# Optimization experiments

Hardware: AMD Instinct MI355X
Metric: run time of the kernel (lower is better)

The kernel has to match this reference:

```python
import jax, jax.numpy as jnp
import numpy as np
from jax import lax

DIM = 64
HEADS = 8
B, H, W = 4, 256, 256


def layer_norm(x, w, b):
    # WithBias LayerNorm over channel dim (dim=1 of NCHW), per-pixel
    mu = jnp.mean(x, axis=1, keepdims=True)
    var = jnp.mean((x - mu) ** 2, axis=1, keepdims=True)
    xn = (x - mu) / jnp.sqrt(var + 1e-5)
    return xn * w[None, :, None, None] + b[None, :, None, None]


def conv1x1(x, w, b=None):
    out = jnp.einsum('oc,bchw->bohw', w, x)
    if b is not None:
        out = out + b[None, :, None, None]
    return out


def dwconv3x3(x, w):
    # w: [C,1,3,3], depthwise (groups=C), stride 1, pad 1
    return lax.conv_general_dilated(
        x, w, window_strides=(1, 1), padding=((1, 1), (1, 1)),
        feature_group_count=x.shape[1],
        dimension_numbers=('NCHW', 'OIHW', 'NCHW'))


def modulation(v, y, mw, mb):
    # mw: [4, C, C] = [scale0, scale1, shift0, shift1]; mb: [4, C]
    s = conv1x1(jax.nn.leaky_relu(conv1x1(y, mw[0], mb[0]), 0.1), mw[1], mb[1])
    t = conv1x1(jax.nn.leaky_relu(conv1x1(y, mw[2], mb[2]), 0.1), mw[3], mb[3])
    return v * (s + 1.0) + t


def _heads(t):
    b, c, h, w = t.shape
    return t.reshape(b, HEADS, c // HEADS, h * w)


def channel_attn(q, k, v, temp):
    b, c, h, w = v.shape
    q, k, v = _heads(q), _heads(k), _heads(v)  # b, head, ch, hw
    q = q / jnp.maximum(jnp.linalg.norm(q, axis=-1, keepdims=True), 1e-12)
    k = k / jnp.maximum(jnp.linalg.norm(k, axis=-1, keepdims=True), 1e-12)
    attn = jnp.einsum('bhcn,bhdn->bhcd', q, k) * temp[None]  # small CxC
    attn = jax.nn.softmax(attn, axis=-1)
    out = jnp.einsum('bhcd,bhdn->bhcn', attn, v)
    return out.reshape(b, c, h, w)


def setup_inputs() -> dict:
    key = jax.random.key(0)
    ks = jax.random.split(key, 24)
    sc = 0.05
    d = {
        'x': jax.random.normal(ks[0], (B, DIM, H, W), jnp.float32),
        'y': jax.random.normal(ks[1], (B, DIM, H, W), jnp.float32),
        'ln_w': jnp.ones((DIM,), jnp.float32),
        'ln_b': jnp.zeros((DIM,), jnp.float32),
        'temp': jnp.ones((HEADS, 1, 1), jnp.float32),
        'kv1_w': jax.random.normal(ks[2], (2 * DIM, DIM), jnp.float32) * sc,
        'kvdw1_w': jax.random.normal(ks[3], (2 * DIM, 1, 3, 3), jnp.float32) * sc,
        'q1_w': jax.random.normal(ks[4], (DIM, DIM), jnp.float32) * sc,
        'qdw1_w': jax.random.normal(ks[5], (DIM, 1, 3, 3), jnp.float32) * sc,
        'po1_w': jax.random.normal(ks[6], (DIM, DIM), jnp.float32) * sc,
        'kv2_w': jax.random.normal(ks[7], (2 * DIM, DIM), jnp.float32) * sc,
        'kvdw2_w': jax.random.normal(ks[8], (2 * DIM, 1, 3, 3), jnp.float32) * sc,
        'q2_w': jax.random.normal(ks[9], (DIM, DIM), jnp.float32) * sc,
        'qdw2_w': jax.random.normal(ks[10], (DIM, 1, 3, 3), jnp.float32) * sc,
        'po2_w': jax.random.normal(ks[11], (DIM, DIM), jnp.float32) * sc,
        'mm1_w': jax.random.normal(ks[12], (4, DIM, DIM), jnp.float32) * sc,
        'mm1_b': jnp.zeros((4, DIM), jnp.float32),
        'mm2_w': jax.random.normal(ks[13], (4, DIM, DIM), jnp.float32) * sc,
        'mm2_b': jnp.zeros((4, DIM), jnp.float32),
    }
    return d


def reference(x, y, ln_w, ln_b, temp,
              kv1_w, kvdw1_w, q1_w, qdw1_w, po1_w,
              kv2_w, kvdw2_w, q2_w, qdw2_w, po2_w,
              mm1_w, mm1_b, mm2_w, mm2_b):
    x1 = layer_norm(x, ln_w, ln_b)
    y1 = layer_norm(y, ln_w, ln_b)  # original reuses self.norm1 for both

    # branch 1: kv from x1, q from y1, v modulated by x, residual y
    kv1 = dwconv3x3(conv1x1(x1, kv1_w), kvdw1_w)
    k1, v1 = jnp.split(kv1, 2, axis=1)
    q1 = dwconv3x3(conv1x1(y1, q1_w), qdw1_w)
    v1 = modulation(v1, x, mm1_w, mm1_b)
    out1 = conv1x1(channel_attn(q1, k1, v1, temp), po1_w) + y

    # branch 2: kv from y1, q from x1, v modulated by y, residual x
    kv2 = dwconv3x3(conv1x1(y1, kv2_w), kvdw2_w)
    k2, v2 = jnp.split(kv2, 2, axis=1)
    q2 = dwconv3x3(conv1x1(x1, q2_w), qdw2_w)
    v2 = modulation(v2, y, mm2_w, mm2_b)
    out2 = conv1x1(channel_attn(q2, k2, v2, temp), po2_w) + x

    return (out1, out2)
```

## Files before the change

kernel.cpp:

```cpp
#include <hip/hip_runtime.h>
#include <hip/hip_bf16.h>

#define HW 65536
#define BATCH 4
#define NPIX (BATCH*HW)

typedef unsigned short u16;
typedef unsigned int   u32;
typedef __attribute__((ext_vector_type(8))) short bh8;
typedef __attribute__((ext_vector_type(4))) float f4;

__device__ __forceinline__ float b2f(u16 u){
    u32 i = ((u32)u) << 16; float f; __builtin_memcpy(&f, &i, 4); return f;
}
__device__ __forceinline__ u16 f2b(float f){
    __hip_bfloat16 h = __float2bfloat16(f); u16 u; __builtin_memcpy(&u, &h, 2); return u;
}

__device__ __forceinline__ f4 mfma16(bh8 a, bh8 b, f4 c){
    return __builtin_amdgcn_mfma_f32_16x16x32_bf16(a, b, c, 0, 0, 0);
}

struct CvtJob { const float* src; u16* dst; int n; const float* cs; };
struct SetupArgs {
    CvtJob j[12];
    const float* kvw[2]; const float* qw[2];
    const float* lnw; const float* lnb;
    float* sums; float* lnc;
};
__global__ __launch_bounds__(256) void setup_kernel(SetupArgs S){
    int blk = blockIdx.x;
    if (blk < 12){
        const CvtJob J = S.j[blk];
        if (J.cs){
            for (int i = threadIdx.x; i < J.n; i += 256) J.dst[i] = f2b(J.src[i] * J.cs[i & 63]);
        } else {
            for (int i = threadIdx.x; i < J.n; i += 256) J.dst[i] = f2b(J.src[i]);
        }
        return;
    }
    int pb = blk - 12;
    if (pb == 0){
        for (int i = threadIdx.x; i < 5120; i += 256) S.sums[i] = 0.f;
    } else if (pb <= 2){
        const float* W = S.kvw[pb-1];
        float* rs = S.lnc + (pb-1)*256;
        int o = threadIdx.x;
        if (o < 128){
            float a = 0.f, bb = 0.f;
            for (int c = 0; c < 64; c++){
                float wv = W[o*64 + c];
                a = fmaf(wv, S.lnw[c], a); bb = fmaf(wv, S.lnb[c], bb);
            }
            rs[o] = a; rs[128 + o] = bb;
        }
    } else {
        const float* W = S.qw[pb-3];
        float* rs = S.lnc + 512 + (pb-3)*128;
        int o = threadIdx.x;
        if (o < 64){
            float a = 0.f, bb = 0.f;
            for (int c = 0; c < 64; c++){
                float wv = W[o*64 + c];
                a = fmaf(wv, S.lnw[c], a); bb = fmaf(wv, S.lnb[c], bb);
            }
            rs[o] = a; rs[64 + o] = bb;
        }
    }
}

struct GemmDual {
    const float* in[2];
    const u16* wa[2];
    const float* rs[2]; const float* rb[2];
    u16* outLo[2]; u16* outHi[2];
};
template<int MT>
__global__ __launch_bounds__(256,4) void gemmln_kernel(GemmDual G){
    constexpr int KD = 64;
    constexpr int NW = MT*16*KD;
    __shared__ u16 wl[NW];
    int seg = blockIdx.x >> 11, tile = blockIdx.x & 2047;
    {
        const u16* W = G.wa[seg];
        for (int i = threadIdx.x; i < NW/8; i += 256){
            int row = i >> 3, ch = i & 7;
            uint4 v = *(const uint4*)(W + row*KD + ch*8);
            *(uint4*)(wl + row*KD + ((ch ^ (row & 7)) << 3)) = v;
        }
    }
    __syncthreads();

    int w = threadIdx.x >> 6, lane = threadIdx.x & 63;
    int quad = lane >> 4, l16 = lane & 15;
    int b = tile >> 9;
    int pbase = ((tile & 511) << 7) + (w << 5) + (l16 << 1);

    f4 acc[MT][2];
    #pragma unroll
    for (int mi = 0; mi < MT; mi++){ acc[mi][0] = (f4){0.f,0.f,0.f,0.f}; acc[mi][1] = (f4){0.f,0.f,0.f,0.f}; }

    float s1a = 0.f, s2a = 0.f, s1b = 0.f, s2b = 0.f;
    #pragma unroll
    for (int ks = 0; ks < 2; ks++){
        const float* pp = G.in[seg] + ((size_t)b*64 + ks*32 + quad*8)*HW + pbase;
        bh8 b0, b1;
        #pragma unroll
        for (int j = 0; j < 8; j++){
            float2 f = *(const float2*)(pp + (size_t)j*HW);
            s1a += f.x; s2a = fmaf(f.x, f.x, s2a);
            s1b += f.y; s2b = fmaf(f.y, f.y, s2b);
            b0[j] = (short)f2b(f.x);
            b1[j] = (short)f2b(f.y);
        }
        #pragma unroll
        for (int mi = 0; mi < MT; mi++){
            bh8 a;
            __builtin_memcpy(&a, wl + (mi*16 + l16)*KD + ((((ks<<2)+quad) ^ (l16 & 7)) << 3), 16);
            acc[mi][0] = mfma16(a, b0, acc[mi][0]);
            acc[mi][1] = mfma16(a, b1, acc[mi][1]);
        }
    }

    s1a += __shfl_xor(s1a, 16); s1a += __shfl_xor(s1a, 32);
    s2a += __shfl_xor(s2a, 16); s2a += __shfl_xor(s2a, 32);
    s1b += __shfl_xor(s1b, 16); s1b += __shfl_xor(s1b, 32);
    s2b += __shfl_xor(s2b, 16); s2b += __shfl_xor(s2b, 32);
    float mu0 = s1a*(1.f/64.f), iv0 = rsqrtf(s2a*(1.f/64.f) - mu0*mu0 + 1e-5f);
    float mu1 = s1b*(1.f/64.f), iv1 = rsqrtf(s2b*(1.f/64.f) - mu1*mu1 + 1e-5f);

    const float* rs = G.rs[seg]; const float* rb = G.rb[seg];
    u16* oLo = G.outLo[seg]; u16* oHi = G.outHi[seg];
    #pragma unroll
    for (int mi = 0; mi < MT; mi++)
    #pragma unroll
    for (int r = 0; r < 4; r++){
        int o = mi*16 + quad*4 + r;
        size_t pidx = ((size_t)b*64 + (o & 63))*HW + pbase;
        float rsv = rs[o], rbv = rb[o];
        float va0 = iv0*(acc[mi][0][r] - mu0*rsv) + rbv;
        float va1 = iv1*(acc[mi][1][r] - mu1*rsv) + rbv;
        u16* dst = (o < 64) ? oLo : oHi;
        *(u32*)(dst + pidx) = (u32)f2b(va0) | ((u32)f2b(va1) << 16);
    }
}

struct DwArgs { const u16* in0; const u16* in1; const u16* in2;
                u16* out0; u16* out1; u16* out2;
                const float* w0; const float* w1; const float* w2;
                int c0, c1, c2; };
__global__ __launch_bounds__(256) void dw3_kernel(DwArgs A){
    int seg = blockIdx.x >> 13;
    int lid = ((blockIdx.x & 8191) << 8) + threadIdx.x;
    const u16* inp = seg == 0 ? A.in0 : seg == 1 ? A.in1 : A.in2;
    u16* outp      = seg == 0 ? A.out0 : seg == 1 ? A.out1 : A.out2;
    const float* wd = seg == 0 ? A.w0 : seg == 1 ? A.w1 : A.w2;
    int choff      = seg == 0 ? A.c0 : seg == 1 ? A.c1 : A.c2;
    int bc = lid >> 13;
    int n8 = lid & 8191;
    int h = n8 >> 5, c8 = (n8 & 31) << 3;
    const float* wc = wd + ((size_t)((bc & 63) + choff))*9;
    const u16* p = inp + (size_t)bc*HW;
    float row[3][10];
    #pragma unroll
    for (int r = 0; r < 3; r++){
        int hh = h - 1 + r;
        bool ok = (unsigned)hh < 256u;
        const u16* pr = p + hh*256 + c8;
        if (ok){
            uint4 m = *(const uint4*)pr;
            row[r][1] = b2f((u16)m.x); row[r][2] = b2f((u16)(m.x>>16));
            row[r][3] = b2f((u16)m.y); row[r][4] = b2f((u16)(m.y>>16));
            row[r][5] = b2f((u16)m.z); row[r][6] = b2f((u16)(m.z>>16));
            row[r][7] = b2f((u16)m.w); row[r][8] = b2f((u16)(m.w>>16));
            row[r][0] = (c8 > 0)   ? b2f(pr[-1]) : 0.f;
            row[r][9] = (c8 < 248) ? b2f(pr[8])  : 0.f;
        } else {
            #pragma unroll
            for (int j = 0; j < 10; j++) row[r][j] = 0.f;
        }
    }
    float o[8];
    #pragma unroll
    for (int i = 0; i < 8; i++){
        float a = 0.f;
        #pragma unroll
        for (int r = 0; r < 3; r++){
            a = fmaf(wc[r*3+0], row[r][i],   a);
            a = fmaf(wc[r*3+1], row[r][i+1], a);
            a = fmaf(wc[r*3+2], row[r][i+2], a);
        }
        o[i] = a;
    }
    uint4 st;
    st.x = (u32)f2b(o[0]) | ((u32)f2b(o[1])<<16);
    st.y = (u32)f2b(o[2]) | ((u32)f2b(o[3])<<16);
    st.z = (u32)f2b(o[4]) | ((u32)f2b(o[5])<<16);
    st.w = (u32)f2b(o[6]) | ((u32)f2b(o[7])<<16);
    *(uint4*)(outp + (size_t)bc*HW + h*256 + c8) = st;
}

#define NSL 64
struct AttnDual { const u16* q[2]; const u16* k[2]; float* sums; };
__global__ __launch_bounds__(256) void attn_part_kernel(AttnDual AD){
    int seg = blockIdx.x >> 11;
    int blk = blockIdx.x & 2047;
    int sl = blk & (NSL-1);
    int bh = blk >> 6;
    int b = bh >> 3, h = bh & 7;
    const u16* qp = AD.q[seg] + ((size_t)b*64 + h*8)*HW + sl*(HW/NSL);
    const u16* kp = AD.k[seg] + ((size_t)b*64 + h*8)*HW + sl*(HW/NSL);
    float acc[80];
    #pragma unroll
    for (int i = 0; i < 80; i++) acc[i] = 0.f;
    int n0 = threadIdx.x << 2;
    float qv[8][4], kw[8][4];
    #pragma unroll
    for (int i = 0; i < 8; i++){
        uint2 mq = *(const uint2*)(qp + (size_t)i*HW + n0);
        uint2 mk = *(const uint2*)(kp + (size_t)i*HW + n0);
        qv[i][0] = b2f((u16)(mq.x & 0xffffu)); qv[i][1] = b2f((u16)(mq.x >> 16));
        qv[i][2] = b2f((u16)(mq.y & 0xffffu)); qv[i][3] = b2f((u16)(mq.y >> 16));
        kw[i][0] = b2f((u16)(mk.x & 0xffffu)); kw[i][1] = b2f((u16)(mk.x >> 16));
        kw[i][2] = b2f((u16)(mk.y & 0xffffu)); kw[i][3] = b2f((u16)(mk.y >> 16));
    }
    #pragma unroll
    for (int i = 0; i < 8; i++){
        #pragma unroll
        for (int u = 0; u < 4; u++){
            acc[64+i] = fmaf(qv[i][u], qv[i][u], acc[64+i]);
            acc[72+i] = fmaf(kw[i][u], kw[i][u], acc[72+i]);
        }
        #pragma unroll
        for (int j = 0; j < 8; j++)
            #pragma unroll
            for (int u = 0; u < 4; u++)
                acc[i*8+j] = fmaf(qv[i][u], kw[j][u], acc[i*8+j]);
    }
    __shared__ float sred[4][80];
    int lane = threadIdx.x & 63, wv = threadIdx.x >> 6;
    #pragma unroll
    for (int t = 0; t < 80; t++){
        float r = acc[t];
        r += __shfl_down(r, 32); r += __shfl_down(r, 16); r += __shfl_down(r, 8);
        r += __shfl_down(r, 4);  r += __shfl_down(r, 2);  r += __shfl_down(r, 1);
        if (lane == 0) sred[wv][t] = r;
    }
    __syncthreads();
    if (threadIdx.x < 80){
        int t = threadIdx.x;
        atomicAdd(&AD.sums[seg*2560 + bh*80 + t], sred[0][t]+sred[1][t]+sred[2][t]+sred[3][t]);
    }
}

struct WeffDual { const float* sums; const float* temp; const float* po[2]; u16* weff[2]; };
__global__ __launch_bounds__(64) void weff_kernel(WeffDual WD){
    int seg = blockIdx.x >> 2;
    int b = blockIdx.x & 3;
    const float* po = WD.po[seg];
    u16* weff = WD.weff[seg];
    __shared__ float at[8][8][8];
    int t = threadIdx.x;
    {
        int h = t >> 3, i = t & 7;
        const float* f = WD.sums + seg*2560 + (b*8 + h)*80;
        float iq = 1.f / fmaxf(sqrtf(f[64+i]), 1e-12f);
        float tv = WD.temp[h];
        float row[8]; float m = -1e30f;
        #pragma unroll
        for (int j = 0; j < 8; j++){
            float ik = 1.f / fmaxf(sqrtf(f[72+j]), 1e-12f);
            row[j] = f[i*8+j]*iq*ik*tv;
            m = fmaxf(m, row[j]);
        }
        float s = 0.f;
        #pragma unroll
        for (int j = 0; j < 8; j++){ row[j] = expf(row[j]-m); s += row[j]; }
        float rsv = 1.f/s;
        #pragma unroll
        for (int j = 0; j < 8; j++) at[h][i][j] = row[j]*rsv;
    }
    __syncthreads();
    int o = t;
    for (int g = 0; g < 64; g++){
        int h = g >> 3, j = g & 7;
        float wv = 0.f;
        #pragma unroll
        for (int i = 0; i < 8; i++) wv = fmaf(po[o*64 + h*8 + i], at[h][i][j], wv);
        weff[b*4096 + o*64 + g] = f2b(wv);
    }
}

struct ModFinal {
    const float* in[2]; const u16* wa[2]; const u16* wb[2];
    const float* b0[2]; const float* b2[2]; const float* b1[2]; const float* b3[2];
    const u16* wf[2];
    const u16* v[2];
    const float* resid[2];
    float* out[2];
};
__global__ __launch_bounds__(256) void modfinal_kernel(ModFinal M){
    __shared__ u32 lds[128*65];
    __shared__ u16 wl[8192];
    int seg = blockIdx.x >> 11, tile = blockIdx.x & 2047;
    int w = threadIdx.x >> 6, lane = threadIdx.x & 63;
    int quad = lane >> 4, l16 = lane & 15;
    int b = tile >> 9;
    int pbase = ((tile & 511) << 7) + (w << 5) + (l16 << 1);
    int pxp = (w << 4) + l16;

    auto loadW = [&](const u16* W, int nrows){
        for (int i = threadIdx.x; i < nrows*8; i += 256){
            int row = i >> 3, ch = i & 7;
            uint4 vv = *(const uint4*)(W + row*64 + ch*8);
            *(uint4*)(wl + row*64 + ((ch ^ (row & 7)) << 3)) = vv;
        }
    };

    loadW(M.wa[seg], 128);
    __syncthreads();
    f4 acc[8][2];
    #pragma unroll
    for (int mi = 0; mi < 8; mi++){ acc[mi][0] = (f4){0.f,0.f,0.f,0.f}; acc[mi][1] = (f4){0.f,0.f,0.f,0.f}; }
    #pragma unroll
    for (int ks = 0; ks < 2; ks++){
        const float* pp = M.in[seg] + ((size_t)b*64 + ks*32 + quad*8)*HW + pbase;
        bh8 f0, f1;
        #pragma unroll
        for (int j = 0; j < 8; j++){
            float2 f = *(const float2*)(pp + (size_t)j*HW);
            f0[j] = (short)f2b(f.x);
            f1[j] = (short)f2b(f.y);
        }
        #pragma unroll
        for (int mi = 0; mi < 8; mi++){
            bh8 a;
            __builtin_memcpy(&a, wl + (mi*16 + l16)*64 + ((((ks<<2)+quad) ^ (l16 & 7)) << 3), 16);
            acc[mi][0] = mfma16(a, f0, acc[mi][0]);
            acc[mi][1] = mfma16(a, f1, acc[mi][1]);
        }
    }
    {
        const float* b0v = M.b0[seg]; const float* b2v = M.b2[seg];
        #pragma unroll
        for (int mi = 0; mi < 8; mi++)
        #pragma unroll
        for (int r = 0; r < 4; r++){
            int o = mi*16 + quad*4 + r;
            float bi = (o < 64) ? b0v[o] : b2v[o-64];
            float v0 = acc[mi][0][r] + bi; v0 = v0 > 0.f ? v0 : 0.1f*v0;
            float v1 = acc[mi][1][r] + bi; v1 = v1 > 0.f ? v1 : 0.1f*v1;
            lds[o*65 + ((pxp + ((o>>2)&3)*4) & 63)] = (u32)f2b(v0) | ((u32)f2b(v1) << 16);
        }
    }
    __syncthreads();

    loadW(M.wb[seg], 128);
    __syncthreads();
    f4 acc2[8][2];
    #pragma unroll
    for (int mi = 0; mi < 8; mi++){ acc2[mi][0] = (f4){0.f,0.f,0.f,0.f}; acc2[mi][1] = (f4){0.f,0.f,0.f,0.f}; }
    #pragma unroll
    for (int ks = 0; ks < 4; ks++){
        int kb = ks*32 + quad*8;
        bh8 bb0, bb1;
        #pragma unroll
        for (int j = 0; j < 8; j++){
            int ch = kb + j;
            u32 m = lds[ch*65 + ((pxp + ((ch>>2)&3)*4) & 63)];
            bb0[j] = (short)(m & 0xffffu);
            bb1[j] = (short)(m >> 16);
        }
        #pragma unroll
        for (int mi = 0; mi < 8; mi++){
            if (mi < 4 ? (ks < 2) : (ks >= 2)){
                int ksl = (mi >= 4) ? ks - 2 : ks;
                bh8 a;
                __builtin_memcpy(&a, wl + (mi*16 + l16)*64 + ((((ksl<<2)+quad) ^ (l16 & 7)) << 3), 16);
                acc2[mi][0] = mfma16(a, bb0, acc2[mi][0]);
                acc2[mi][1] = mfma16(a, bb1, acc2[mi][1]);
            }
        }
    }
    __syncthreads();

    loadW(M.wf[seg] + b*4096, 64);
    {
        const float* b1v = M.b1[seg]; const float* b3v = M.b3[seg];
        const u16* vP = M.v[seg];
        #pragma unroll
        for (int mi = 0; mi < 4; mi++)
        #pragma unroll
        for (int r = 0; r < 4; r++){
            int o = mi*16 + quad*4 + r;
            size_t pidx = ((size_t)b*64 + o)*HW + pbase;
            float s0 = acc2[mi][0][r] + b1v[o];
            float s1 = acc2[mi][1][r] + b1v[o];
            float t0 = acc2[mi+4][0][r] + b3v[o];
            float t1 = acc2[mi+4][1][r] + b3v[o];
            u32 vv = *(const u32*)(vP + pidx);
            float v0 = b2f((u16)(vv & 0xffffu)), v1 = b2f((u16)(vv >> 16));
            lds[o*65 + ((pxp + ((o>>2)&3)*4) & 63)] = (u32)f2b(v0*(s0+1.f)+t0)
                                                    | ((u32)f2b(v1*(s1+1.f)+t1) << 16);
        }
    }
    __syncthreads();

    f4 accF[4][2];
    #pragma unroll
    for (int mi = 0; mi < 4; mi++){ accF[mi][0] = (f4){0.f,0.f,0.f,0.f}; accF[mi][1] = (f4){0.f,0.f,0.f,0.f}; }
    #pragma unroll
    for (int ks = 0; ks < 2; ks++){
        int kb = ks*32 + quad*8;
        bh8 bb0, bb1;
        #pragma unroll
        for (int j = 0; j < 8; j++){
            int ch = kb + j;
            u32 m = lds[ch*65 + ((pxp + ((ch>>2)&3)*4) & 63)];
            bb0[j] = (short)(m & 0xffffu);
            bb1[j] = (short)(m >> 16);
        }
        #pragma unroll
        for (int mi = 0; mi < 4; mi++){
            bh8 a;
            __builtin_memcpy(&a, wl + (mi*16 + l16)*64 + ((((ks<<2)+quad) ^ (l16 & 7)) << 3), 16);
            accF[mi][0] = mfma16(a, bb0, accF[mi][0]);
            accF[mi][1] = mfma16(a, bb1, accF[mi][1]);
        }
    }
    {
        const float* resid = M.resid[seg];
        float* outF = M.out[seg];
        #pragma unroll
        for (int mi = 0; mi < 4; mi++)
        #pragma unroll
        for (int r = 0; r < 4; r++){
            int o = mi*16 + quad*4 + r;
            size_t pidx = ((size_t)b*64 + o)*HW + pbase;
            float2 rr = *(const float2*)(resid + pidx);
            float2 st; st.x = accF[mi][0][r] + rr.x; st.y = accF[mi][1][r] + rr.y;
            *(float2*)(outF + pidx) = st;
        }
    }
}

extern "C" void kernel_launch(void* const* d_in, const int* in_sizes, int n_in,
                              void* d_out, int out_size, void* d_ws, size_t ws_size,
                              hipStream_t stream){
    const float* x    = (const float*)d_in[0];
    const float* y    = (const float*)d_in[1];
    const float* ln_w = (const float*)d_in[2];
    const float* ln_b = (const float*)d_in[3];
    const float* temp = (const float*)d_in[4];
    const float* kv_w[2]   = {(const float*)d_in[5],  (const float*)d_in[10]};
    const float* kvdw_w[2] = {(const float*)d_in[6],  (const float*)d_in[11]};
    const float* q_w[2]    = {(const float*)d_in[7],  (const float*)d_in[12]};
    const float* qdw_w[2]  = {(const float*)d_in[8],  (const float*)d_in[13]};
    const float* po_w[2]   = {(const float*)d_in[9],  (const float*)d_in[14]};
    const float* mm_w[2]   = {(const float*)d_in[15], (const float*)d_in[17]};
    const float* mm_b[2]   = {(const float*)d_in[16], (const float*)d_in[18]};

    const size_t HPE = (size_t)BATCH*64*HW;
    u16* PL = (u16*)d_ws;
    u16* P[9];
    for (int i = 0; i < 9; i++) P[i] = PL + (size_t)i*HPE;
    float* sums = (float*)(PL + 9*HPE);
    float* lnc  = sums + 5120;
    u16* warena = (u16*)(lnc + 768);
    const int WKV[2] = {0, 8192}, WQ[2] = {16384, 20480};
    const int WMA[2] = {24576, 40960}, WMB[2] = {32768, 49152};
    const int WEFF[2] = {57344, 73728};

    size_t need = 9*HPE*2 + (5120+768)*4 + 90112*2;
    if (ws_size < need) return;

    SetupArgs S{};
    int nj = 0;
    auto add = [&](const float* s, u16* d, int n, const float* cs){ S.j[nj] = {s, d, n, cs}; nj++; };
    for (int br = 0; br < 2; br++){
        add(kv_w[br],        warena + WKV[br],        8192, ln_w);
        add(q_w[br],         warena + WQ[br],         4096, ln_w);
        add(mm_w[br],        warena + WMA[br],        4096, nullptr);
        add(mm_w[br]+8192,   warena + WMA[br] + 4096, 4096, nullptr);
        add(mm_w[br]+4096,   warena + WMB[br],        4096, nullptr);
        add(mm_w[br]+12288,  warena + WMB[br] + 4096, 4096, nullptr);
    }
    S.kvw[0] = kv_w[0]; S.kvw[1] = kv_w[1];
    S.qw[0]  = q_w[0];  S.qw[1]  = q_w[1];
    S.lnw = ln_w; S.lnb = ln_b; S.sums = sums; S.lnc = lnc;
    setup_kernel<<<17, 256, 0, stream>>>(S);

    const int GT = NPIX/128;

    GemmDual GK{};
    GK.in[0] = x; GK.in[1] = y;
    GK.wa[0] = warena + WKV[0]; GK.wa[1] = warena + WKV[1];
    GK.rs[0] = lnc;        GK.rb[0] = lnc + 128;
    GK.rs[1] = lnc + 256;  GK.rb[1] = lnc + 384;
    GK.outLo[0] = P[0]; GK.outHi[0] = P[1];
    GK.outLo[1] = P[3]; GK.outHi[1] = P[4];
    gemmln_kernel<8><<<2*GT, 256, 0, stream>>>(GK);

    GemmDual GQ{};
    GQ.in[0] = y; GQ.in[1] = x;
    GQ.wa[0] = warena + WQ[0]; GQ.wa[1] = warena + WQ[1];
    GQ.rs[0] = lnc + 512;  GQ.rb[0] = lnc + 576;
    GQ.rs[1] = lnc + 640;  GQ.rb[1] = lnc + 704;
    GQ.outLo[0] = P[2]; GQ.outHi[0] = P[2];
    GQ.outLo[1] = P[5]; GQ.outHi[1] = P[5];
    gemmln_kernel<4><<<2*GT, 256, 0, stream>>>(GQ);

    DwArgs D0{P[0], P[1], P[2], P[6], P[7], P[8],
              kvdw_w[0], kvdw_w[0], qdw_w[0], 0, 64, 0};
    dw3_kernel<<<3*8192, 256, 0, stream>>>(D0);
    DwArgs D1{P[3], P[4], P[5], P[0], P[1], P[2],
              kvdw_w[1], kvdw_w[1], qdw_w[1], 0, 64, 0};
    dw3_kernel<<<3*8192, 256, 0, stream>>>(D1);

    AttnDual AD{};
    AD.q[0] = P[8]; AD.k[0] = P[6];
    AD.q[1] = P[2]; AD.k[1] = P[0];
    AD.sums = sums;
    attn_part_kernel<<<2*BATCH*8*NSL, 256, 0, stream>>>(AD);

    WeffDual WD{};
    WD.sums = sums; WD.temp = temp;
    WD.po[0] = po_w[0]; WD.po[1] = po_w[1];
    WD.weff[0] = warena + WEFF[0]; WD.weff[1] = warena + WEFF[1];
    weff_kernel<<<2*BATCH, 64, 0, stream>>>(WD);

    float* outp = (float*)d_out;
    ModFinal M{};
    M.in[0] = x; M.in[1] = y;
    M.wa[0] = warena + WMA[0]; M.wa[1] = warena + WMA[1];
    M.wb[0] = warena + WMB[0]; M.wb[1] = warena + WMB[1];
    M.b0[0] = mm_b[0];       M.b0[1] = mm_b[1];
    M.b2[0] = mm_b[0] + 128; M.b2[1] = mm_b[1] + 128;
    M.b1[0] = mm_b[0] + 64;  M.b1[1] = mm_b[1] + 64;
    M.b3[0] = mm_b[0] + 192; M.b3[1] = mm_b[1] + 192;
    M.wf[0] = warena + WEFF[0]; M.wf[1] = warena + WEFF[1];
    M.v[0] = P[7]; M.v[1] = P[1];
    M.resid[0] = y; M.resid[1] = x;
    M.out[0] = outp; M.out[1] = outp + HPE;
    modfinal_kernel<<<2*GT, 256, 0, stream>>>(M);
}
```

Baseline: 741.5 us.

## Prefetch inputs early, read weights from global, merge depthwise launches

The LN-GEMM kernel now issues all input loads before staging weights into LDS, so global latency overlaps the weight copy. The modulation/final kernel drops its LDS weight staging and reads MFMA A-fragments straight from global/L1. It also double-buffers the input loads and prefetches the v and residual values ahead of the syncs, and shrinks the padded LDS tile to 128x64 with a new swizzle so it can run at higher occupancy. The two depthwise launches become one six-segment launch, which needs three more workspace planes and reassigned buffers. The trade-off is more register pressure from the prefetch arrays and uncoalesced global weight reads.

```diff
diff --git a/kernel.cpp b/kernel.cpp
--- a/kernel.cpp
+++ b/kernel.cpp
@@ -81,6 +81,19 @@
     constexpr int NW = MT*16*KD;
     __shared__ u16 wl[NW];
     int seg = blockIdx.x >> 11, tile = blockIdx.x & 2047;
+    int w = threadIdx.x >> 6, lane = threadIdx.x & 63;
+    int quad = lane >> 4, l16 = lane & 15;
+    int b = tile >> 9;
+    int pbase = ((tile & 511) << 7) + (w << 5) + (l16 << 1);
+
+    const float* in = G.in[seg];
+    float2 f[16];
+    #pragma unroll
+    for (int ks = 0; ks < 2; ks++)
+        #pragma unroll
+        for (int j = 0; j < 8; j++)
+            f[ks*8+j] = *(const float2*)(in + ((size_t)b*64 + ks*32 + quad*8 + j)*HW + pbase);
+
     {
         const u16* W = G.wa[seg];
         for (int i = threadIdx.x; i < NW/8; i += 256){
@@ -91,36 +104,31 @@
     }
     __syncthreads();
 
-    int w = threadIdx.x >> 6, lane = threadIdx.x & 63;
-    int quad = lane >> 4, l16 = lane & 15;
-    int b = tile >> 9;
-    int pbase = ((tile & 511) << 7) + (w << 5) + (l16 << 1);
+    float s1a = 0.f, s2a = 0.f, s1b = 0.f, s2b = 0.f;
+    bh8 b0[2], b1[2];
+    #pragma unroll
+    for (int ks = 0; ks < 2; ks++)
+        #pragma unroll
+        for (int j = 0; j < 8; j++){
+            float2 fv = f[ks*8+j];
+            s1a += fv.x; s2a = fmaf(fv.x, fv.x, s2a);
+            s1b += fv.y; s2b = fmaf(fv.y, fv.y, s2b);
+            b0[ks][j] = (short)f2b(fv.x);
+            b1[ks][j] = (short)f2b(fv.y);
+        }
 
     f4 acc[MT][2];
     #pragma unroll
     for (int mi = 0; mi < MT; mi++){ acc[mi][0] = (f4){0.f,0.f,0.f,0.f}; acc[mi][1] = (f4){0.f,0.f,0.f,0.f}; }
-
-    float s1a = 0.f, s2a = 0.f, s1b = 0.f, s2b = 0.f;
-    #pragma unroll
-    for (int ks = 0; ks < 2; ks++){
-        const float* pp = G.in[seg] + ((size_t)b*64 + ks*32 + quad*8)*HW + pbase;
-        bh8 b0, b1;
-        #pragma unroll
-        for (int j = 0; j < 8; j++){
-            float2 f = *(const float2*)(pp + (size_t)j*HW);
-            s1a += f.x; s2a = fmaf(f.x, f.x, s2a);
-            s1b += f.y; s2b = fmaf(f.y, f.y, s2b);
-            b0[j] = (short)f2b(f.x);
-            b1[j] = (short)f2b(f.y);
-        }
+    #pragma unroll
+    for (int ks = 0; ks < 2; ks++)
         #pragma unroll
         for (int mi = 0; mi < MT; mi++){
             bh8 a;
             __builtin_memcpy(&a, wl + (mi*16 + l16)*KD + ((((ks<<2)+quad) ^ (l16 & 7)) << 3), 16);
-            acc[mi][0] = mfma16(a, b0, acc[mi][0]);
-            acc[mi][1] = mfma16(a, b1, acc[mi][1]);
-        }
-    }
+            acc[mi][0] = mfma16(a, b0[ks], acc[mi][0]);
+            acc[mi][1] = mfma16(a, b1[ks], acc[mi][1]);
+        }
 
     s1a += __shfl_xor(s1a, 16); s1a += __shfl_xor(s1a, 32);
     s2a += __shfl_xor(s2a, 16); s2a += __shfl_xor(s2a, 32);
@@ -145,17 +153,14 @@
     }
 }
 
-struct DwArgs { const u16* in0; const u16* in1; const u16* in2;
-                u16* out0; u16* out1; u16* out2;
-                const float* w0; const float* w1; const float* w2;
-                int c0, c1, c2; };
-__global__ __launch_bounds__(256) void dw3_kernel(DwArgs A){
+struct Dw6 { const u16* in[6]; u16* out[6]; const float* w[6]; int choff[6]; };
+__global__ __launch_bounds__(256) void dw6_kernel(Dw6 A){
     int seg = blockIdx.x >> 13;
     int lid = ((blockIdx.x & 8191) << 8) + threadIdx.x;
-    const u16* inp = seg == 0 ? A.in0 : seg == 1 ? A.in1 : A.in2;
-    u16* outp      = seg == 0 ? A.out0 : seg == 1 ? A.out1 : A.out2;
-    const float* wd = seg == 0 ? A.w0 : seg == 1 ? A.w1 : A.w2;
-    int choff      = seg == 0 ? A.c0 : seg == 1 ? A.c1 : A.c2;
+    const u16* inp = A.in[seg];
+    u16* outp      = A.out[seg];
+    const float* wd = A.w[seg];
+    int choff      = A.choff[seg];
     int bc = lid >> 13;
     int n8 = lid & 8191;
     int h = n8 >> 5, c8 = (n8 & 31) << 3;
@@ -299,9 +304,8 @@
     const float* resid[2];
     float* out[2];
 };
-__global__ __launch_bounds__(256) void modfinal_kernel(ModFinal M){
-    __shared__ u32 lds[128*65];
-    __shared__ u16 wl[8192];
+__global__ __launch_bounds__(256,4) void modfinal_kernel(ModFinal M){
+    __shared__ u32 lds[128*64];
     int seg = blockIdx.x >> 11, tile = blockIdx.x & 2047;
     int w = threadIdx.x >> 6, lane = threadIdx.x & 63;
     int quad = lane >> 4, l16 = lane & 15;
@@ -309,37 +313,53 @@
     int pbase = ((tile & 511) << 7) + (w << 5) + (l16 << 1);
     int pxp = (w << 4) + l16;
 
-    auto loadW = [&](const u16* W, int nrows){
-        for (int i = threadIdx.x; i < nrows*8; i += 256){
-            int row = i >> 3, ch = i & 7;
-            uint4 vv = *(const uint4*)(W + row*64 + ch*8);
-            *(uint4*)(wl + row*64 + ((ch ^ (row & 7)) << 3)) = vv;
-        }
-    };
-
-    loadW(M.wa[seg], 128);
-    __syncthreads();
+    const float* in = M.in[seg];
+    const u16* wa = M.wa[seg];
+
+    float2 f[8];
+    #pragma unroll
+    for (int j = 0; j < 8; j++)
+        f[j] = *(const float2*)(in + ((size_t)b*64 + quad*8 + j)*HW + pbase);
+
     f4 acc[8][2];
     #pragma unroll
     for (int mi = 0; mi < 8; mi++){ acc[mi][0] = (f4){0.f,0.f,0.f,0.f}; acc[mi][1] = (f4){0.f,0.f,0.f,0.f}; }
+
     #pragma unroll
     for (int ks = 0; ks < 2; ks++){
-        const float* pp = M.in[seg] + ((size_t)b*64 + ks*32 + quad*8)*HW + pbase;
+        float2 fn[8];
+        if (ks == 0){
+            #pragma unroll
+            for (int j = 0; j < 8; j++)
+                fn[j] = *(const float2*)(in + ((size_t)b*64 + 32 + quad*8 + j)*HW + pbase);
+        }
         bh8 f0, f1;
         #pragma unroll
         for (int j = 0; j < 8; j++){
-            float2 f = *(const float2*)(pp + (size_t)j*HW);
-            f0[j] = (short)f2b(f.x);
-            f1[j] = (short)f2b(f.y);
+            f0[j] = (short)f2b(f[j].x);
+            f1[j] = (short)f2b(f[j].y);
         }
         #pragma unroll
         for (int mi = 0; mi < 8; mi++){
             bh8 a;
-            __builtin_memcpy(&a, wl + (mi*16 + l16)*64 + ((((ks<<2)+quad) ^ (l16 & 7)) << 3), 16);
+            __builtin_memcpy(&a, wa + (mi*16 + l16)*64 + ks*32 + quad*8, 16);
             acc[mi][0] = mfma16(a, f0, acc[mi][0]);
             acc[mi][1] = mfma16(a, f1, acc[mi][1]);
         }
-    }
+        #pragma unroll
+        for (int j = 0; j < 8; j++) f[j] = fn[j];
+    }
+
+    u32 vpref[16];
+    {
+        const u16* vP = M.v[seg];
+        #pragma unroll
+        for (int mi = 0; mi < 4; mi++)
+        #pragma unroll
+        for (int r = 0; r < 4; r++)
+            vpref[mi*4+r] = *(const u32*)(vP + ((size_t)b*64 + mi*16 + quad*4 + r)*HW + pbase);
+    }
+
     {
         const float* b0v = M.b0[seg]; const float* b2v = M.b2[seg];
         #pragma unroll
@@ -350,13 +370,12 @@
             float bi = (o < 64) ? b0v[o] : b2v[o-64];
             float v0 = acc[mi][0][r] + bi; v0 = v0 > 0.f ? v0 : 0.1f*v0;
             float v1 = acc[mi][1][r] + bi; v1 = v1 > 0.f ? v1 : 0.1f*v1;
-            lds[o*65 + ((pxp + ((o>>2)&3)*4) & 63)] = (u32)f2b(v0) | ((u32)f2b(v1) << 16);
+            lds[o*64 + ((pxp + ((o>>2)&3)*8) & 63)] = (u32)f2b(v0) | ((u32)f2b(v1) << 16);
         }
     }
     __syncthreads();
 
-    loadW(M.wb[seg], 128);
-    __syncthreads();
+    const u16* wb = M.wb[seg];
     f4 acc2[8][2];
     #pragma unroll
     for (int mi = 0; mi < 8; mi++){ acc2[mi][0] = (f4){0.f,0.f,0.f,0.f}; acc2[mi][1] = (f4){0.f,0.f,0.f,0.f}; }
@@ -367,7 +386,7 @@
         #pragma unroll
         for (int j = 0; j < 8; j++){
             int ch = kb + j;
-            u32 m = lds[ch*65 + ((pxp + ((ch>>2)&3)*4) & 63)];
+            u32 m = lds[ch*64 + ((pxp + ((ch>>2)&3)*8) & 63)];
             bb0[j] = (short)(m & 0xffffu);
             bb1[j] = (short)(m >> 16);
         }
@@ -376,7 +395,7 @@
             if (mi < 4 ? (ks < 2) : (ks >= 2)){
                 int ksl = (mi >= 4) ? ks - 2 : ks;
                 bh8 a;
-                __builtin_memcpy(&a, wl + (mi*16 + l16)*64 + ((((ksl<<2)+quad) ^ (l16 & 7)) << 3), 16);
+                __builtin_memcpy(&a, wb + (mi*16 + l16)*64 + ksl*32 + quad*8, 16);
                 acc2[mi][0] = mfma16(a, bb0, acc2[mi][0]);
                 acc2[mi][1] = mfma16(a, bb1, acc2[mi][1]);
             }
@@ -384,28 +403,35 @@
     }
     __syncthreads();
 
-    loadW(M.wf[seg] + b*4096, 64);
     {
         const float* b1v = M.b1[seg]; const float* b3v = M.b3[seg];
-        const u16* vP = M.v[seg];
         #pragma unroll
         for (int mi = 0; mi < 4; mi++)
         #pragma unroll
         for (int r = 0; r < 4; r++){
             int o = mi*16 + quad*4 + r;
-            size_t pidx = ((size_t)b*64 + o)*HW + pbase;
             float s0 = acc2[mi][0][r] + b1v[o];
             float s1 = acc2[mi][1][r] + b1v[o];
             float t0 = acc2[mi+4][0][r] + b3v[o];
             float t1 = acc2[mi+4][1][r] + b3v[o];
-            u32 vv = *(const u32*)(vP + pidx);
+            u32 vv = vpref[mi*4+r];
             float v0 = b2f((u16)(vv & 0xffffu)), v1 = b2f((u16)(vv >> 16));
-            lds[o*65 + ((pxp + ((o>>2)&3)*4) & 63)] = (u32)f2b(v0*(s0+1.f)+t0)
+            lds[o*64 + ((pxp + ((o>>2)&3)*8) & 63)] = (u32)f2b(v0*(s0+1.f)+t0)
                                                     | ((u32)f2b(v1*(s1+1.f)+t1) << 16);
         }
     }
+    float2 rpre[16];
+    {
+        const float* resid = M.resid[seg];
+        #pragma unroll
+        for (int mi = 0; mi < 4; mi++)
+        #pragma unroll
+        for (int r = 0; r < 4; r++)
+            rpre[mi*4+r] = *(const float2*)(resid + ((size_t)b*64 + mi*16 + quad*4 + r)*HW + pbase);
+    }
     __syncthreads();
 
+    const u16* wf = M.wf[seg] + b*4096;
     f4 accF[4][2];
     #pragma unroll
     for (int mi = 0; mi < 4; mi++){ accF[mi][0] = (f4){0.f,0.f,0.f,0.f}; accF[mi][1] = (f4){0.f,0.f,0.f,0.f}; }
@@ -416,20 +442,19 @@
         #pragma unroll
         for (int j = 0; j < 8; j++){
             int ch = kb + j;
-            u32 m = lds[ch*65 + ((pxp + ((ch>>2)&3)*4) & 63)];
+            u32 m = lds[ch*64 + ((pxp + ((ch>>2)&3)*8) & 63)];
             bb0[j] = (short)(m & 0xffffu);
             bb1[j] = (short)(m >> 16);
         }
         #pragma unroll
         for (int mi = 0; mi < 4; mi++){
             bh8 a;
-            __builtin_memcpy(&a, wl + (mi*16 + l16)*64 + ((((ks<<2)+quad) ^ (l16 & 7)) << 3), 16);
+            __builtin_memcpy(&a, wf + (mi*16 + l16)*64 + ks*32 + quad*8, 16);
             accF[mi][0] = mfma16(a, bb0, accF[mi][0]);
             accF[mi][1] = mfma16(a, bb1, accF[mi][1]);
         }
     }
     {
-        const float* resid = M.resid[seg];
         float* outF = M.out[seg];
         #pragma unroll
         for (int mi = 0; mi < 4; mi++)
@@ -437,7 +462,7 @@
         for (int r = 0; r < 4; r++){
             int o = mi*16 + quad*4 + r;
             size_t pidx = ((size_t)b*64 + o)*HW + pbase;
-            float2 rr = *(const float2*)(resid + pidx);
+            float2 rr = rpre[mi*4+r];
             float2 st; st.x = accF[mi][0][r] + rr.x; st.y = accF[mi][1][r] + rr.y;
             *(float2*)(outF + pidx) = st;
         }
@@ -462,16 +487,16 @@
 
     const size_t HPE = (size_t)BATCH*64*HW;
     u16* PL = (u16*)d_ws;
-    u16* P[9];
-    for (int i = 0; i < 9; i++) P[i] = PL + (size_t)i*HPE;
-    float* sums = (float*)(PL + 9*HPE);
+    u16* P[12];
+    for (int i = 0; i < 12; i++) P[i] = PL + (size_t)i*HPE;
+    float* sums = (float*)(PL + 12*HPE);
     float* lnc  = sums + 5120;
     u16* warena = (u16*)(lnc + 768);
     const int WKV[2] = {0, 8192}, WQ[2] = {16384, 20480};
     const int WMA[2] = {24576, 40960}, WMB[2] = {32768, 49152};
     const int WEFF[2] = {57344, 73728};
 
-    size_t need = 9*HPE*2 + (5120+768)*4 + 90112*2;
+    size_t need = 12*HPE*2 + (5120+768)*4 + 90112*2;
     if (ws_size < need) return;
 
     SetupArgs S{};
@@ -498,7 +523,7 @@
     GK.rs[0] = lnc;        GK.rb[0] = lnc + 128;
     GK.rs[1] = lnc + 256;  GK.rb[1] = lnc + 384;
     GK.outLo[0] = P[0]; GK.outHi[0] = P[1];
-    GK.outLo[1] = P[3]; GK.outHi[1] = P[4];
+    GK.outLo[1] = P[2]; GK.outHi[1] = P[3];
     gemmln_kernel<8><<<2*GT, 256, 0, stream>>>(GK);
 
     GemmDual GQ{};
@@ -506,20 +531,22 @@
     GQ.wa[0] = warena + WQ[0]; GQ.wa[1] = warena + WQ[1];
     GQ.rs[0] = lnc + 512;  GQ.rb[0] = lnc + 576;
     GQ.rs[1] = lnc + 640;  GQ.rb[1] = lnc + 704;
-    GQ.outLo[0] = P[2]; GQ.outHi[0] = P[2];
+    GQ.outLo[0] = P[4]; GQ.outHi[0] = P[4];
     GQ.outLo[1] = P[5]; GQ.outHi[1] = P[5];
     gemmln_kernel<4><<<2*GT, 256, 0, stream>>>(GQ);
 
-    DwArgs D0{P[0], P[1], P[2], P[6], P[7], P[8],
-              kvdw_w[0], kvdw_w[0], qdw_w[0], 0, 64, 0};
-    dw3_kernel<<<3*8192, 256, 0, stream>>>(D0);
-    DwArgs D1{P[3], P[4], P[5], P[0], P[1], P[2],
-              kvdw_w[1], kvdw_w[1], qdw_w[1], 0, 64, 0};
-    dw3_kernel<<<3*8192, 256, 0, stream>>>(D1);
+    Dw6 D{};
+    D.in[0] = P[0];  D.out[0] = P[6];  D.w[0] = kvdw_w[0]; D.choff[0] = 0;
+    D.in[1] = P[1];  D.out[1] = P[7];  D.w[1] = kvdw_w[0]; D.choff[1] = 64;
+    D.in[2] = P[4];  D.out[2] = P[8];  D.w[2] = qdw_w[0];  D.choff[2] = 0;
+    D.in[3] = P[2];  D.out[3] = P[9];  D.w[3] = kvdw_w[1]; D.choff[3] = 0;
+    D.in[4] = P[3];  D.out[4] = P[10]; D.w[4] = kvdw_w[1]; D.choff[4] = 64;
+    D.in[5] = P[5];  D.out[5] = P[11]; D.w[5] = qdw_w[1];  D.choff[5] = 0;
+    dw6_kernel<<<6*8192, 256, 0, stream>>>(D);
 
     AttnDual AD{};
-    AD.q[0] = P[8]; AD.k[0] = P[6];
-    AD.q[1] = P[2]; AD.k[1] = P[0];
+    AD.q[0] = P[8];  AD.k[0] = P[6];
+    AD.q[1] = P[11]; AD.k[1] = P[9];
     AD.sums = sums;
     attn_part_kernel<<<2*BATCH*8*NSL, 256, 0, stream>>>(AD);
 
@@ -539,7 +566,7 @@
     M.b1[0] = mm_b[0] + 64;  M.b1[1] = mm_b[1] + 64;
     M.b3[0] = mm_b[0] + 192; M.b3[1] = mm_b[1] + 192;
     M.wf[0] = warena + WEFF[0]; M.wf[1] = warena + WEFF[1];
-    M.v[0] = P[7]; M.v[1] = P[1];
+    M.v[0] = P[7]; M.v[1] = P[10];
     M.resid[0] = y; M.resid[1] = x;
     M.out[0] = outp; M.out[1] = outp + HPE;
     modfinal_kernel<<<2*GT, 256, 0, stream>>>(M);
```

After: 721.4 us. 1.03x faster.
